# Optimization experiments

Measured on AMD Instinct MI355X. Metric: run time of the kernel, lower is better.

The kernel has to match this reference:

```python
import jax, jax.numpy as jnp
import numpy as np


def setup_inputs() -> dict:
    key = jax.random.key(0)
    ks = jax.random.split(key, 6)
    B, S, H = 1, 512, 2048
    NH, D = 16, 128
    S_CACHE = 8192
    TOPK = 16
    hidden_states = jax.random.normal(ks[0], (B, S, H), dtype=jnp.float32)
    Wqkv = jax.random.normal(ks[1], (3 * H, H), dtype=jnp.float32) * 0.02
    Wout = jax.random.normal(ks[2], (H, H), dtype=jnp.float32) * 0.02
    k_cache = jax.random.normal(ks[3], (B, NH, S_CACHE, D), dtype=jnp.float32)
    v_cache = jax.random.normal(ks[4], (B, NH, S_CACHE, D), dtype=jnp.float32)
    position_bias = jax.random.normal(ks[5], (NH, S, S), dtype=jnp.float32) * 0.1
    # causal mask: True = masked out (matches torch masked_fill semantics)
    attention_mask = ~jnp.tril(jnp.ones((S, S), dtype=bool))
    return {
        "hidden_states": hidden_states,
        "Wqkv": Wqkv,
        "Wout": Wout,
        "k_cache": k_cache,
        "v_cache": v_cache,
        "position_bias": position_bias,
        "attention_mask": attention_mask,
        "topk": TOPK,
    }


SIM_THRESHOLD = 0.25  # config.sim_threshold


def reference(hidden_states, Wqkv, Wout, k_cache, v_cache, position_bias,
              attention_mask, topk):
    B, S, H = hidden_states.shape
    NH, D = k_cache.shape[1], k_cache.shape[3]
    scale = 1.0 / jnp.sqrt(jnp.asarray(D, hidden_states.dtype))

    # QKV projection (Linear, no bias): x @ W^T, then split heads
    qkv = jnp.einsum('bsh,oh->bso', hidden_states, Wqkv)
    q, k, v = jnp.split(qkv, 3, axis=-1)
    def to_heads(x):
        return x.reshape(B, S, NH, D).transpose(0, 2, 1, 3)  # [B,NH,S,D]
    q, k, v = to_heads(q), to_heads(k), to_heads(v)

    # local attention scores + alibi-style bias
    scores_local = jnp.einsum('bhqd,bhkd->bhqk', q, k) * scale
    scores_local = scores_local + position_bias[None]  # [B,NH,S,S]

    # cosine-similarity retrieval over long-range cache
    q_n = q / jnp.linalg.norm(q, axis=-1, keepdims=True)
    k_n = k_cache / jnp.linalg.norm(k_cache, axis=-1, keepdims=True)
    sim = jnp.einsum('bhqd,bhkd->bhqk', q_n, k_n)  # [B,NH,S,S_CACHE]
    val, idx = jax.lax.top_k(sim, topk)            # [B,NH,S,topk]
    reshaped_idx = idx.reshape(B, NH, S * topk)

    # gather retrieved K/V
    sel_k = jnp.take_along_axis(k_cache, reshaped_idx[..., None], axis=2)  # [B,NH,S*topk,D]
    sel_v = jnp.take_along_axis(v_cache, reshaped_idx[..., None], axis=2)

    scores_cache = jnp.einsum('bhqd,bhkd->bhqk', q, sel_k) * scale  # [B,NH,S,S*topk]
    neg = jnp.finfo(scores_cache.dtype).min

    # similarity-threshold mask (mask_by_sim=True)
    sim_mask = ~(val > SIM_THRESHOLD)                       # [B,NH,S,topk]
    sim_mask = sim_mask.reshape(B, NH, 1, S * topk)         # broadcast over queries
    scores_cache = jnp.where(sim_mask, neg, scores_cache)

    # block-diagonal external-memory mask: query i attends only to its own topk slots
    rows = jnp.arange(S)[:, None]
    cols_block = jnp.arange(S * topk)[None, :] // topk
    ext_mask = cols_block != rows                           # [S, S*topk], True = masked

    full_mask = jnp.concatenate([ext_mask, attention_mask], axis=1)  # [S, S*topk+S]
    scores = jnp.concatenate([scores_cache, scores_local], axis=-1)
    scores = jnp.where(full_mask[None, None], neg, scores)

    attn = jax.nn.softmax(scores.astype(jnp.float32), axis=-1).astype(v.dtype)
    values = jnp.concatenate([sel_v, v], axis=2)            # [B,NH,S*topk+S,D]
    ctx = jnp.einsum('bhqk,bhkd->bhqd', attn, values)
    ctx = ctx.transpose(0, 2, 1, 3).reshape(B, S, H)
    attn_output = jnp.einsum('bsh,oh->bso', ctx, Wout)
    return attn_output
```

## Files before the change

### kernel.cpp

```cpp
#include <hip/hip_runtime.h>

typedef _Float16 half8 __attribute__((ext_vector_type(8)));
typedef _Float16 half4 __attribute__((ext_vector_type(4)));
typedef _Float16 half2t __attribute__((ext_vector_type(2)));
typedef float f32x4 __attribute__((ext_vector_type(4)));
typedef float f32x2 __attribute__((ext_vector_type(2)));

#define NHEAD 16
#define SEQ 512
#define DIM 128
#define HID 2048
#define SCACHE 8192
#define CAP 64
#define SCALE 0.08838834764831845f
#define NEG_INF (-__builtin_inff())
#define RECMAX 512

__global__ __launch_bounds__(256) void gemm_xwT(const float* __restrict__ A,
                                                const float* __restrict__ B,
                                                float* __restrict__ Cpart,
                                                int K, int gridN, int kslices) {
  __shared__ __align__(16) _Float16 As[128][84];
  __shared__ __align__(16) _Float16 Bs[128][84];
  int b = blockIdx.x;
  int kblk = b % kslices;
  int nm = b / kslices;
  int nblk = nm % gridN, mblk = nm / gridN;
  int N = gridN * 128;
  int kchunk = K / kslices;
  int t = threadIdx.x;
  int lane = t & 63, wid = t >> 6;
  int wm = (wid >> 1) * 64, wn = (wid & 1) * 64;
  f32x4 acc[4][4] = {};
  const float* Ab = A + (size_t)mblk * 128 * K;
  const float* Bb = B + (size_t)nblk * 128 * K;
  int rowS = t >> 4, c4 = (t & 15) * 4;

  for (int k0 = kblk * kchunk; k0 < kblk * kchunk + kchunk; k0 += 64) {
#pragma unroll
    for (int i = 0; i < 8; ++i) {
      int row = rowS + 16 * i;
      float4 av = *(const float4*)(Ab + (size_t)row * K + k0 + c4);
      float4 bv = *(const float4*)(Bb + (size_t)row * K + k0 + c4);
      half4 ah = {(_Float16)av.x, (_Float16)av.y, (_Float16)av.z, (_Float16)av.w};
      half4 bh = {(_Float16)bv.x, (_Float16)bv.y, (_Float16)bv.z, (_Float16)bv.w};
      *(half4*)&As[row][c4] = ah;
      *(half4*)&Bs[row][c4] = bh;
    }
    __syncthreads();
#pragma unroll
    for (int ks = 0; ks < 2; ++ks) {
      int ko = ks * 32 + (lane >> 4) * 8;
      int rr = lane & 15;
      half8 af[4], bf[4];
#pragma unroll
      for (int i = 0; i < 4; ++i) af[i] = *(const half8*)&As[wm + i * 16 + rr][ko];
#pragma unroll
      for (int j = 0; j < 4; ++j) bf[j] = *(const half8*)&Bs[wn + j * 16 + rr][ko];
#pragma unroll
      for (int i = 0; i < 4; ++i)
#pragma unroll
        for (int j = 0; j < 4; ++j)
          acc[i][j] = __builtin_amdgcn_mfma_f32_16x16x32_f16(af[i], bf[j], acc[i][j], 0, 0, 0);
    }
    __syncthreads();
  }
  float* Cp = Cpart + (size_t)kblk * ((size_t)gridN * 128) * 512;
  int cR = (lane >> 4) * 4, cC = lane & 15;
#pragma unroll
  for (int i = 0; i < 4; ++i)
#pragma unroll
    for (int j = 0; j < 4; ++j) {
      int row = mblk * 128 + wm + i * 16 + cR;
      int col = nblk * 128 + wn + j * 16 + cC;
#pragma unroll
      for (int r = 0; r < 4; ++r)
        Cp[(size_t)(row + r) * N + col] = acc[i][j][r];
    }
}

__global__ __launch_bounds__(256) void reduce_k(const float* __restrict__ part,
                                                float* __restrict__ dst,
                                                int kslices, int ncol, int dstride) {
  size_t e = ((size_t)blockIdx.x * 256 + threadIdx.x) * 4;
  size_t slice = (size_t)512 * ncol;
  f32x4 s = *(const f32x4*)(part + e);
  for (int p = 1; p < kslices; ++p)
    s += *(const f32x4*)(part + (size_t)p * slice + e);
  size_t row = e / ncol;
  int col = (int)(e % ncol);
  *(f32x4*)(dst + row * dstride + col) = s;
}

__global__ __launch_bounds__(256) void split_hilo(const float* __restrict__ src,
                                                  _Float16* __restrict__ hi,
                                                  _Float16* __restrict__ lo) {
  size_t e = ((size_t)blockIdx.x * 256 + threadIdx.x) * 4;
  f32x4 v = *(const f32x4*)(src + e);
  half4 h = {(_Float16)v[0], (_Float16)v[1], (_Float16)v[2], (_Float16)v[3]};
  half4 l = {(_Float16)(v[0] - (float)h[0]), (_Float16)(v[1] - (float)h[1]),
             (_Float16)(v[2] - (float)h[2]), (_Float16)(v[3] - (float)h[3])};
  *(half4*)(hi + e) = h;
  *(half4*)(lo + e) = l;
}

__global__ __launch_bounds__(256) void gemm_q_hi(const _Float16* __restrict__ Ahg,
                                                 const _Float16* __restrict__ Alg,
                                                 const _Float16* __restrict__ Bhg,
                                                 const _Float16* __restrict__ Blg,
                                                 float* __restrict__ C) {
  __shared__ __align__(16) _Float16 Ahs[32][72], Als[32][72];
  __shared__ __align__(16) _Float16 Bhs[32][72], Bls[32][72];
  int b = blockIdx.x;
  int nblk = b & 63, mblk = b >> 6;
  int t = threadIdx.x, lane = t & 63, w = t >> 6;
  int wm = (w >> 1) * 16, wn = (w & 1) * 16;
  int quad = lane >> 4, rr = lane & 15;
  f32x4 acc = {};
  const _Float16* Ab0 = Ahg + (size_t)(mblk * 32) * 2048;
  const _Float16* Ab1 = Alg + (size_t)(mblk * 32) * 2048;
  const _Float16* Bb0 = Bhg + (size_t)(nblk * 32) * 2048;
  const _Float16* Bb1 = Blg + (size_t)(nblk * 32) * 2048;
  int srow = t >> 3, sc = (t & 7) * 8;

  for (int k0 = 0; k0 < 2048; k0 += 64) {
    size_t goff = (size_t)srow * 2048 + k0 + sc;
    *(uint4*)&Ahs[srow][sc] = *(const uint4*)(Ab0 + goff);
    *(uint4*)&Als[srow][sc] = *(const uint4*)(Ab1 + goff);
    *(uint4*)&Bhs[srow][sc] = *(const uint4*)(Bb0 + goff);
    *(uint4*)&Bls[srow][sc] = *(const uint4*)(Bb1 + goff);
    __syncthreads();
#pragma unroll
    for (int ks = 0; ks < 2; ++ks) {
      int ko = ks * 32 + quad * 8;
      half8 afh = *(const half8*)&Ahs[wm + rr][ko];
      half8 afl = *(const half8*)&Als[wm + rr][ko];
      half8 bfh = *(const half8*)&Bhs[wn + rr][ko];
      half8 bfl = *(const half8*)&Bls[wn + rr][ko];
      acc = __builtin_amdgcn_mfma_f32_16x16x32_f16(afl, bfh, acc, 0, 0, 0);
      acc = __builtin_amdgcn_mfma_f32_16x16x32_f16(afh, bfl, acc, 0, 0, 0);
      acc = __builtin_amdgcn_mfma_f32_16x16x32_f16(afh, bfh, acc, 0, 0, 0);
    }
    __syncthreads();
  }
  int row = mblk * 32 + wm + quad * 4;
  int col = nblk * 32 + wn + rr;
#pragma unroll
  for (int r = 0; r < 4; ++r)
    C[(size_t)(row + r) * (3 * HID) + col] = acc[r];
}

__global__ __launch_bounds__(256) void cache_norm(const float* __restrict__ kc,
                                                  _Float16* __restrict__ kn16,
                                                  double* __restrict__ kninv) {
  int w = threadIdx.x >> 6, lane = threadIdx.x & 63;
  int row = blockIdx.x * 4 + w;
  f32x2 v = *(const f32x2*)(kc + (size_t)row * DIM + lane * 2);
  double s = (double)v[0] * v[0] + (double)v[1] * v[1];
#pragma unroll
  for (int off = 32; off; off >>= 1) s += __shfl_xor(s, off);
  float inv = rsqrtf((float)s);
  half2t o = {(_Float16)(v[0] * inv), (_Float16)(v[1] * inv)};
  *(half2t*)(kn16 + (size_t)row * DIM + lane * 2) = o;
  if (lane == 0) kninv[row] = 1.0 / sqrt(s);
}

__global__ __launch_bounds__(256) void prep_local(const float* __restrict__ qkv,
                                                  _Float16* __restrict__ q16,
                                                  _Float16* __restrict__ k16,
                                                  _Float16* __restrict__ qn16) {
  int w = threadIdx.x >> 6, lane = threadIdx.x & 63;
  int rid = blockIdx.x * 4 + w;
  int h = rid >> 9, s = rid & 511;
  const float* qp = qkv + (size_t)s * (3 * HID) + h * DIM + lane * 2;
  f32x2 q = *(const f32x2*)qp;
  f32x2 k = *(const f32x2*)(qp + HID);
  float ss = q[0] * q[0] + q[1] * q[1];
#pragma unroll
  for (int off = 32; off; off >>= 1) ss += __shfl_xor(ss, off);
  float inv = rsqrtf(ss);
  half2t qh = {(_Float16)q[0], (_Float16)q[1]};
  half2t kh = {(_Float16)k[0], (_Float16)k[1]};
  half2t qnh = {(_Float16)(q[0] * inv), (_Float16)(q[1] * inv)};
  *(half2t*)(q16 + (size_t)rid * DIM + lane * 2) = qh;
  *(half2t*)(k16 + (size_t)rid * DIM + lane * 2) = kh;
  *(half2t*)(qn16 + (size_t)rid * DIM + lane * 2) = qnh;
}

__global__ __launch_bounds__(256) void sim_cand(const _Float16* __restrict__ qn16,
                                                const _Float16* __restrict__ kn16,
                                                int* __restrict__ rec,
                                                int* __restrict__ reccnt) {
  __shared__ __align__(16) _Float16 As[128 * 128];
  __shared__ int ls_buf[RECMAX];
  __shared__ int ls_cnt;
  int b = blockIdx.x;
  int xcd = b & 7, slot = b >> 3;
  int mq = slot & 3;
  int p = (slot >> 2) * 8 + xcd;
  int h = p >> 6, nblk = p & 63;
  int t = threadIdx.x, lane = t & 63, w = t >> 6;
  int quad = lane >> 4, rr = lane & 15;
  if (t == 0) ls_cnt = 0;

  half8 bf[2][4];
  {
    const _Float16* kb = kn16 + ((size_t)(h * SCACHE + nblk * 128 + w * 32)) * DIM;
#pragma unroll
    for (int jn = 0; jn < 2; ++jn)
#pragma unroll
      for (int ks = 0; ks < 4; ++ks)
        bf[jn][ks] = *(const half8*)(kb + (size_t)(jn * 16 + rr) * DIM + ks * 32 + quad * 8);
  }

  {
    const _Float16* qA = qn16 + ((size_t)(h * SEQ + mq * 128)) * DIM;
    uint4 sreg[8];
#pragma unroll
    for (int i = 0; i < 8; ++i) {
      int f = t + 256 * i;
      sreg[i] = *(const uint4*)(qA + (size_t)(f >> 4) * DIM + (f & 15) * 8);
    }
#pragma unroll
    for (int i = 0; i < 8; ++i) {
      int f = t + 256 * i;
      int row = f >> 4, c = f & 15;
      *(uint4*)&As[row * DIM + ((c ^ (row & 7)) * 8)] = sreg[i];
    }
  }
  __syncthreads();

  f32x4 acc[8][2] = {};
#pragma unroll
  for (int i = 0; i < 8; ++i) {
    int R = i * 16 + rr;
    half8 af[4];
#pragma unroll
    for (int ks = 0; ks < 4; ++ks)
      af[ks] = *(const half8*)&As[R * DIM + (((ks * 4 + quad) ^ (rr & 7)) * 8)];
#pragma unroll
    for (int jn = 0; jn < 2; ++jn)
#pragma unroll
      for (int ks = 0; ks < 4; ++ks)
        acc[i][jn] = __builtin_amdgcn_mfma_f32_16x16x32_f16(af[ks], bf[jn][ks], acc[i][jn], 0, 0, 0);
  }

#pragma unroll
  for (int i = 0; i < 8; ++i)
#pragma unroll
    for (int jn = 0; jn < 2; ++jn)
#pragma unroll
      for (int r = 0; r < 4; ++r) {
        float v = acc[i][jn][r];
        if (v > 0.249f) {
          int q = mq * 128 + i * 16 + quad * 4 + r;
          int key = nblk * 128 + w * 32 + jn * 16 + rr;
          int pq = atomicAdd(&ls_cnt, 1);
          if (pq < RECMAX) ls_buf[pq] = (q << 13) | key;
        }
      }
  __syncthreads();
  int total = ls_cnt;
  if (total > RECMAX) total = RECMAX;
  int* rp = rec + (size_t)b * RECMAX;
  for (int e = t; e < total; e += 256) rp[e] = ls_buf[e];
  if (t == 0) reccnt[b] = total;
}

__global__ __launch_bounds__(256) void cand_merge(const int* __restrict__ rec,
                                                  const int* __restrict__ reccnt,
                                                  int* __restrict__ cnt,
                                                  int* __restrict__ cidx) {
  __shared__ int lc[128];
  __shared__ int pfx[65];
  __shared__ int bAs[64];
  int blk = blockIdx.x;
  int h = blk >> 2, mq = blk & 3;
  int t = threadIdx.x;
  if (t < 128) lc[t] = 0;
  if (t < 64) {
    int p = h * 64 + t;
    int bA = (p & 7) + 8 * (((p >> 3) << 2) + mq);
    bAs[t] = bA;
    pfx[t + 1] = reccnt[bA];
  }
  if (t == 0) pfx[0] = 0;
  __syncthreads();
  if (t == 0) {
    int s = 0;
    for (int i = 1; i <= 64; ++i) { s += pfx[i]; pfx[i] = s; }
  }
  __syncthreads();
  int T = pfx[64];

  for (int e0 = t; e0 < T; e0 += 512) {
    int e1 = e0 + 256;
    int lo0 = 0, hi0 = 64;
#pragma unroll
    for (int it = 0; it < 6; ++it) {
      int mid = (lo0 + hi0) >> 1;
      if (pfx[mid] <= e0) lo0 = mid; else hi0 = mid;
    }
    int lo1 = 0;
    if (e1 < T) {
      int hi1 = 64;
#pragma unroll
      for (int it = 0; it < 6; ++it) {
        int mid = (lo1 + hi1) >> 1;
        if (pfx[mid] <= e1) lo1 = mid; else hi1 = mid;
      }
    }
    int rv0 = rec[(size_t)bAs[lo0] * RECMAX + (e0 - pfx[lo0])];
    int rv1 = (e1 < T) ? rec[(size_t)bAs[lo1] * RECMAX + (e1 - pfx[lo1])] : 0;

    {
      int q = rv0 >> 13, key = rv0 & 8191;
      int pos = atomicAdd(&lc[q & 127], 1);
      if (pos < CAP) cidx[((size_t)h * 512 + q) * CAP + pos] = key;
    }
    if (e1 < T) {
      int q = rv1 >> 13, key = rv1 & 8191;
      int pos = atomicAdd(&lc[q & 127], 1);
      if (pos < CAP) cidx[((size_t)h * 512 + q) * CAP + pos] = key;
    }
  }
  __syncthreads();
  if (t < 128) cnt[h * 512 + mq * 128 + t] = lc[t];
}

__global__ __launch_bounds__(256) void select_topk(const int* __restrict__ cnt,
                                                   const int* __restrict__ cidx,
                                                   const float* __restrict__ qkv,
                                                   const float* __restrict__ kcache,
                                                   const double* __restrict__ kninv,
                                                   int* __restrict__ sel_idx,
                                                   float* __restrict__ sel_score) {
  int w = threadIdx.x >> 6, lane = threadIdx.x & 63;
  int rowid = blockIdx.x * 4 + w;
  int h = rowid >> 9, s = rowid & 511;
  const float* qp = qkv + (size_t)s * (3 * HID) + h * DIM;

  f32x2 qv2 = *(const f32x2*)(qp + lane * 2);
  double qs = (double)qv2[0] * qv2[0] + (double)qv2[1] * qv2[1];
#pragma unroll
  for (int off = 32; off; off >>= 1) qs += __shfl_xor(qs, off);
  double thr = 0.25 * sqrt(qs);

  int n = min(cnt[rowid], CAP);
  int idx = 0x7fffffff;
  double r = -1e300, d = 0.0;
  if (lane < n) {
    idx = cidx[rowid * CAP + lane];
    const float* kp = kcache + ((size_t)(h * SCACHE + idx)) * DIM;
    double d0 = 0.0, d1 = 0.0;
#pragma unroll
    for (int j = 0; j < DIM; j += 8) {
      f32x4 ka = *(const f32x4*)(kp + j);
      f32x4 kb = *(const f32x4*)(kp + j + 4);
      f32x4 qa = *(const f32x4*)(qp + j);
      f32x4 qb = *(const f32x4*)(qp + j + 4);
      d0 = fma((double)qa[0], (double)ka[0], d0);
      d1 = fma((double)qa[1], (double)ka[1], d1);
      d0 = fma((double)qa[2], (double)ka[2], d0);
      d1 = fma((double)qa[3], (double)ka[3], d1);
      d0 = fma((double)qb[0], (double)kb[0], d0);
      d1 = fma((double)qb[1], (double)kb[1], d1);
      d0 = fma((double)qb[2], (double)kb[2], d0);
      d1 = fma((double)qb[3], (double)kb[3], d1);
    }
    d = d0 + d1;
    r = d * kninv[h * SCACHE + idx];
  }

  int rank = 0;
  for (int j = 0; j < n; ++j) {
    double rj = __shfl(r, j);
    int ij = __shfl(idx, j);
    if (rj > r || (rj == r && ij < idx)) ++rank;
  }
  bool sel = (lane < n) && (rank < 16) && (r > thr);
  unsigned long long m = __ballot(sel);
  int nsel = __popcll(m);
  if (sel) {
    int pos = __popcll(m & ((1ull << lane) - 1));
    sel_idx[rowid * 16 + pos] = idx;
    sel_score[rowid * 16 + pos] = (float)(d * (double)SCALE);
  }
  if (lane >= nsel && lane < 16) {
    sel_idx[rowid * 16 + lane] = 0;
    sel_score[rowid * 16 + lane] = NEG_INF;
  }
}

__global__ __launch_bounds__(256) void attn_part(const float* __restrict__ qkv,
                                                 const _Float16* __restrict__ q16,
                                                 const _Float16* __restrict__ k16,
                                                 const float* __restrict__ bias,
                                                 float* __restrict__ part_m,
                                                 float* __restrict__ part_l,
                                                 float* __restrict__ part_o) {
  __shared__ __align__(16) _Float16 Vs[128][136];
  __shared__ __align__(16) _Float16 Ps[16][136];
  __shared__ float mred[16][4], lred[16][4];

  int pb = blockIdx.x;
  int tt = pb % 80, h = pb / 80;
  int qb, cb;
  if (tt < 8)       { qb = tt;                cb = 0; }
  else if (tt < 24) { int u = tt - 8;  qb = 8 + (u >> 1); cb = u & 1; }
  else if (tt < 48) { int u = tt - 24; int q3 = u / 3; qb = 16 + q3; cb = u - q3 * 3; }
  else              { int u = tt - 48; qb = 24 + (u >> 2); cb = u & 3; }
  int q0 = qb * 16, kc0 = cb * 128;

  int t = threadIdx.x, lane = t & 63, w = t >> 6;
  int quad = lane >> 4, col = lane & 15;

  const float* vbase = qkv + 2 * HID + h * DIM;
#pragma unroll
  for (int i = 0; i < 16; ++i) {
    int idx = t + 256 * i;
    int key = idx & 127, dg = idx >> 7;
    f32x4 vv = *(const f32x4*)(vbase + (size_t)(kc0 + key) * (3 * HID) + dg * 4);
#pragma unroll
    for (int e = 0; e < 4; ++e) Vs[dg * 4 + e][key] = (_Float16)vv[e];
  }

  const _Float16* qbp = q16 + ((size_t)(h * SEQ + q0)) * DIM;
  half8 af[4];
#pragma unroll
  for (int ks = 0; ks < 4; ++ks)
    af[ks] = *(const half8*)(qbp + (size_t)col * DIM + ks * 32 + quad * 8);

  f32x4 acc[2] = {};
#pragma unroll
  for (int jn = 0; jn < 2; ++jn) {
    const _Float16* kp = k16 + ((size_t)(h * SEQ + kc0 + w * 32 + jn * 16 + col)) * DIM;
#pragma unroll
    for (int ks = 0; ks < 4; ++ks) {
      half8 bf = *(const half8*)(kp + ks * 32 + quad * 8);
      acc[jn] = __builtin_amdgcn_mfma_f32_16x16x32_f16(af[ks], bf, acc[jn], 0, 0, 0);
    }
  }
  float s[2][4];
#pragma unroll
  for (int jn = 0; jn < 2; ++jn) {
    int keyg = kc0 + w * 32 + jn * 16 + col;
#pragma unroll
    for (int r = 0; r < 4; ++r) {
      int qrow = q0 + quad * 4 + r;
      float sv = NEG_INF;
      if (keyg <= qrow)
        sv = acc[jn][r] * SCALE + bias[((size_t)h * SEQ + qrow) * SEQ + keyg];
      s[jn][r] = sv;
    }
  }

  float mw[4];
#pragma unroll
  for (int r = 0; r < 4; ++r) {
    float m = fmaxf(s[0][r], s[1][r]);
#pragma unroll
    for (int off = 1; off < 16; off <<= 1) m = fmaxf(m, __shfl_xor(m, off));
    mw[r] = m;
  }
  if (col == 0)
#pragma unroll
    for (int r = 0; r < 4; ++r) mred[quad * 4 + r][w] = mw[r];
  __syncthreads();

  float M[4];
#pragma unroll
  for (int r = 0; r < 4; ++r) {
    int row = quad * 4 + r;
    float m = fmaxf(fmaxf(mred[row][0], mred[row][1]),
                    fmaxf(mred[row][2], mred[row][3]));
    M[r] = m;
    float p0 = __expf(s[0][r] - m);
    float p1 = __expf(s[1][r] - m);
    Ps[row][w * 32 + col] = (_Float16)p0;
    Ps[row][w * 32 + 16 + col] = (_Float16)p1;
    float l = p0 + p1;
#pragma unroll
    for (int off = 1; off < 16; off <<= 1) l += __shfl_xor(l, off);
    if (col == 0) lred[row][w] = l;
  }
  if (w == 0 && col == 0)
#pragma unroll
    for (int r = 0; r < 4; ++r) part_m[pb * 16 + quad * 4 + r] = M[r];
  __syncthreads();

  f32x4 o[2] = {};
#pragma unroll
  for (int jn = 0; jn < 2; ++jn) {
#pragma unroll
    for (int ks = 0; ks < 4; ++ks) {
      half8 a = *(const half8*)&Ps[col][ks * 32 + quad * 8];
      half8 bv = *(const half8*)&Vs[w * 32 + jn * 16 + col][ks * 32 + quad * 8];
      o[jn] = __builtin_amdgcn_mfma_f32_16x16x32_f16(a, bv, o[jn], 0, 0, 0);
    }
  }
#pragma unroll
  for (int jn = 0; jn < 2; ++jn)
#pragma unroll
    for (int r = 0; r < 4; ++r)
      part_o[((size_t)pb * 16 + quad * 4 + r) * 128 + w * 32 + jn * 16 + col] = o[jn][r];
  if (t < 16)
    part_l[pb * 16 + t] = lred[t][0] + lred[t][1] + lred[t][2] + lred[t][3];
}

__global__ __launch_bounds__(256) void attn_merge(const float* __restrict__ part_m,
                                                  const float* __restrict__ part_l,
                                                  const float* __restrict__ part_o,
                                                  const int* __restrict__ sel_idx,
                                                  const float* __restrict__ sel_score,
                                                  const float* __restrict__ vcache,
                                                  float* __restrict__ ctx) {
  int w = threadIdx.x >> 6, lane = threadIdx.x & 63;
  int row = blockIdx.x * 4 + w;
  int h = row >> 9, q = row & 511;
  int qb = q >> 4, r = q & 15;
  int base = (qb < 8) ? qb
           : (qb < 16) ? 8 + 2 * (qb - 8)
           : (qb < 24) ? 24 + 3 * (qb - 16)
                       : 48 + 4 * (qb - 24);
  int ncb = (qb >> 3) + 1;
  int pb0 = h * 80 + base;

  float scv[16], mc = NEG_INF;
#pragma unroll
  for (int j = 0; j < 16; ++j) {
    scv[j] = sel_score[row * 16 + j];
    mc = fmaxf(mc, scv[j]);
  }
  float mi[4];
  float M = mc;
  for (int i = 0; i < ncb; ++i) {
    mi[i] = part_m[(pb0 + i) * 16 + r];
    M = fmaxf(M, mi[i]);
  }
  f32x2 O = {0.f, 0.f};
  float L = 0.f;
  for (int i = 0; i < ncb; ++i) {
    float sc = __expf(mi[i] - M);
    f32x2 ov = *(const f32x2*)(part_o + ((size_t)(pb0 + i) * 16 + r) * 128 + lane * 2);
    O += ov * sc;
    L += part_l[(pb0 + i) * 16 + r] * sc;
  }
#pragma unroll
  for (int j = 0; j < 16; ++j) {
    if (scv[j] > NEG_INF) {
      float wv = __expf(scv[j] - M);
      int idx = sel_idx[row * 16 + j];
      f32x2 v = *(const f32x2*)(vcache + ((size_t)(h * SCACHE + idx)) * DIM + lane * 2);
      O += v * wv;
      L += wv;
    }
  }
  f32x2 res = O * (1.f / L);
  *(f32x2*)(ctx + (size_t)q * HID + h * DIM + lane * 2) = res;
}

extern "C" void kernel_launch(void* const* d_in, const int* in_sizes, int n_in,
                              void* d_out, int out_size, void* d_ws, size_t ws_size,
                              hipStream_t stream) {
  const float* hidden = (const float*)d_in[0];
  const float* Wqkv   = (const float*)d_in[1];
  const float* Wout   = (const float*)d_in[2];
  const float* kcache = (const float*)d_in[3];
  const float* vcache = (const float*)d_in[4];
  const float* bias   = (const float*)d_in[5];

  char* ws = (char*)d_ws;
  size_t off = 0;
  float*    qkv   = (float*)(ws + off);    off += (size_t)SEQ * 3 * HID * 4;
  _Float16* q16   = (_Float16*)(ws + off); off += (size_t)NHEAD * SEQ * DIM * 2;
  _Float16* k16   = (_Float16*)(ws + off); off += (size_t)NHEAD * SEQ * DIM * 2;
  _Float16* qn16  = (_Float16*)(ws + off); off += (size_t)NHEAD * SEQ * DIM * 2;
  _Float16* kn16  = (_Float16*)(ws + off); off += (size_t)NHEAD * SCACHE * DIM * 2;
  double*   kninv = (double*)(ws + off);   off += (size_t)NHEAD * SCACHE * 8;
  int*      ccnt  = (int*)(ws + off);      off += (size_t)NHEAD * SEQ * 4;
  int*      cidx  = (int*)(ws + off);      off += (size_t)NHEAD * SEQ * CAP * 4;
  int*      selidx  = (int*)(ws + off);    off += (size_t)NHEAD * SEQ * 16 * 4;
  float*    selsc   = (float*)(ws + off);  off += (size_t)NHEAD * SEQ * 16 * 4;
  float*    ctx   = (float*)(ws + off);    off += (size_t)SEQ * HID * 4;
  float*    pm    = (float*)(ws + off);    off += (size_t)1280 * 16 * 4;
  float*    pl    = (float*)(ws + off);    off += (size_t)1280 * 16 * 4;
  float*    po    = (float*)(ws + off);    off += (size_t)1280 * 16 * 128 * 4;
  int*      rec    = (int*)po;
  int*      reccnt = rec + (size_t)4096 * RECMAX;
  float*    gpart = (float*)(ws + off);
  _Float16* Ahg = (_Float16*)gpart;
  _Float16* Alg = Ahg + (size_t)SEQ * HID;
  _Float16* Bhg = Alg + (size_t)SEQ * HID;
  _Float16* Blg = Bhg + (size_t)HID * HID;

  cache_norm<<<dim3(NHEAD * SCACHE / 4), dim3(256), 0, stream>>>(kcache, kn16, kninv);
  gemm_xwT<<<dim3(4 * 32 * 4), dim3(256), 0, stream>>>(hidden, Wqkv + (size_t)2048 * 2048,
                                                       gpart, 2048, 32, 4);
  reduce_k<<<dim3(SEQ * 4096 / 1024), dim3(256), 0, stream>>>(gpart, qkv + 2048, 4, 4096,
                                                              3 * HID);
  split_hilo<<<dim3(SEQ * HID / 1024), dim3(256), 0, stream>>>(hidden, Ahg, Alg);
  split_hilo<<<dim3(HID * HID / 1024), dim3(256), 0, stream>>>(Wqkv, Bhg, Blg);
  gemm_q_hi<<<dim3(1024), dim3(256), 0, stream>>>(Ahg, Alg, Bhg, Blg, qkv);
  prep_local<<<dim3(NHEAD * SEQ / 4), dim3(256), 0, stream>>>(qkv, q16, k16, qn16);
  sim_cand<<<dim3(4096), dim3(256), 0, stream>>>(qn16, kn16, rec, reccnt);
  cand_merge<<<dim3(64), dim3(256), 0, stream>>>(rec, reccnt, ccnt, cidx);
  select_topk<<<dim3(NHEAD * SEQ / 4), dim3(256), 0, stream>>>(ccnt, cidx, qkv, kcache,
                                                               kninv, selidx, selsc);
  attn_part<<<dim3(16 * 80), dim3(256), 0, stream>>>(qkv, q16, k16, bias, pm, pl, po);
  attn_merge<<<dim3(NHEAD * SEQ / 4), dim3(256), 0, stream>>>(pm, pl, po, selidx, selsc,
                                                              vcache, ctx);
  gemm_xwT<<<dim3(4 * 16 * 8), dim3(256), 0, stream>>>(ctx, Wout, gpart, 2048, 16, 8);
  reduce_k<<<dim3(SEQ * 2048 / 1024), dim3(256), 0, stream>>>(gpart, (float*)d_out, 8, 2048,
                                                              2048);
}
```

Before: 419.2 us.

## Process four key tiles per sim_cand block with prefetched B fragments

Each sim_cand block now covers 512 cache keys instead of 128, so the Q tile staged in shared memory is reused across four key tiles. The next tile's K fragments are prefetched into registers while the current tile runs its MFMAs. Threshold hits are gathered into a bitmask and walked with ctz instead of 64 branched atomics. The grid shrinks 4x and RECMAX doubles, with cand_merge updated to merge 16 records per head-quarter; the costs are fewer blocks for latency hiding and more register pressure.

```diff
diff --git a/kernel.cpp b/kernel.cpp
--- a/kernel.cpp
+++ b/kernel.cpp
@@ -14,7 +14,7 @@
 #define CAP 64
 #define SCALE 0.08838834764831845f
 #define NEG_INF (-__builtin_inff())
-#define RECMAX 512
+#define RECMAX 1024
 
 __global__ __launch_bounds__(256) void gemm_xwT(const float* __restrict__ A,
                                                 const float* __restrict__ B,
@@ -198,20 +198,23 @@
   int xcd = b & 7, slot = b >> 3;
   int mq = slot & 3;
   int p = (slot >> 2) * 8 + xcd;
-  int h = p >> 6, nblk = p & 63;
+  int h = p >> 4, g = p & 15;
   int t = threadIdx.x, lane = t & 63, w = t >> 6;
   int quad = lane >> 4, rr = lane & 15;
   if (t == 0) ls_cnt = 0;
 
-  half8 bf[2][4];
-  {
-    const _Float16* kb = kn16 + ((size_t)(h * SCACHE + nblk * 128 + w * 32)) * DIM;
+  const _Float16* kbase = kn16 + (size_t)h * SCACHE * DIM
+                        + (size_t)(g * 512 + w * 32 + rr) * DIM + quad * 8;
+  auto loadB = [&](half8 (&dst)[2][4], int tt) {
 #pragma unroll
     for (int jn = 0; jn < 2; ++jn)
 #pragma unroll
       for (int ks = 0; ks < 4; ++ks)
-        bf[jn][ks] = *(const half8*)(kb + (size_t)(jn * 16 + rr) * DIM + ks * 32 + quad * 8);
-  }
+        dst[jn][ks] = *(const half8*)(kbase + (size_t)(tt * 128 + jn * 16) * DIM + ks * 32);
+  };
+
+  half8 bf[2][4], bn[2][4];
+  loadB(bf, 0);
 
   {
     const _Float16* qA = qn16 + ((size_t)(h * SEQ + mq * 128)) * DIM;
@@ -230,35 +233,51 @@
   }
   __syncthreads();
 
-  f32x4 acc[8][2] = {};
-#pragma unroll
-  for (int i = 0; i < 8; ++i) {
-    int R = i * 16 + rr;
-    half8 af[4];
-#pragma unroll
-    for (int ks = 0; ks < 4; ++ks)
-      af[ks] = *(const half8*)&As[R * DIM + (((ks * 4 + quad) ^ (rr & 7)) * 8)];
-#pragma unroll
-    for (int jn = 0; jn < 2; ++jn)
+#pragma unroll
+  for (int tt = 0; tt < 4; ++tt) {
+    if (tt < 3) loadB(bn, tt + 1);
+
+    f32x4 acc[8][2] = {};
+#pragma unroll
+    for (int i = 0; i < 8; ++i) {
+      int R = i * 16 + rr;
+      half8 af[4];
 #pragma unroll
       for (int ks = 0; ks < 4; ++ks)
-        acc[i][jn] = __builtin_amdgcn_mfma_f32_16x16x32_f16(af[ks], bf[jn][ks], acc[i][jn], 0, 0, 0);
-  }
-
-#pragma unroll
-  for (int i = 0; i < 8; ++i)
-#pragma unroll
-    for (int jn = 0; jn < 2; ++jn)
-#pragma unroll
-      for (int r = 0; r < 4; ++r) {
-        float v = acc[i][jn][r];
-        if (v > 0.249f) {
-          int q = mq * 128 + i * 16 + quad * 4 + r;
-          int key = nblk * 128 + w * 32 + jn * 16 + rr;
-          int pq = atomicAdd(&ls_cnt, 1);
-          if (pq < RECMAX) ls_buf[pq] = (q << 13) | key;
-        }
-      }
+        af[ks] = *(const half8*)&As[R * DIM + (((ks * 4 + quad) ^ (rr & 7)) * 8)];
+#pragma unroll
+      for (int jn = 0; jn < 2; ++jn)
+#pragma unroll
+        for (int ks = 0; ks < 4; ++ks)
+          acc[i][jn] = __builtin_amdgcn_mfma_f32_16x16x32_f16(af[ks], bf[jn][ks], acc[i][jn], 0, 0, 0);
+    }
+
+    unsigned long long hm = 0ull;
+#pragma unroll
+    for (int i = 0; i < 8; ++i)
+#pragma unroll
+      for (int jn = 0; jn < 2; ++jn)
+#pragma unroll
+        for (int r = 0; r < 4; ++r)
+          hm |= (unsigned long long)(acc[i][jn][r] > 0.249f) << (i * 8 + jn * 4 + r);
+    int key_base = (g * 4 + tt) * 128 + w * 32 + rr;
+    while (hm) {
+      int bit = __builtin_ctzll(hm);
+      hm &= hm - 1;
+      int i = bit >> 3, jn = (bit >> 2) & 1, r = bit & 3;
+      int q = mq * 128 + i * 16 + (quad << 2) + r;
+      int pq = atomicAdd(&ls_cnt, 1);
+      if (pq < RECMAX) ls_buf[pq] = (q << 13) | (key_base + jn * 16);
+    }
+
+    if (tt < 3) {
+#pragma unroll
+      for (int jn = 0; jn < 2; ++jn)
+#pragma unroll
+        for (int ks = 0; ks < 4; ++ks)
+          bf[jn][ks] = bn[jn][ks];
+    }
+  }
   __syncthreads();
   int total = ls_cnt;
   if (total > RECMAX) total = RECMAX;
@@ -272,14 +291,14 @@
                                                   int* __restrict__ cnt,
                                                   int* __restrict__ cidx) {
   __shared__ int lc[128];
-  __shared__ int pfx[65];
-  __shared__ int bAs[64];
+  __shared__ int pfx[17];
+  __shared__ int bAs[16];
   int blk = blockIdx.x;
   int h = blk >> 2, mq = blk & 3;
   int t = threadIdx.x;
   if (t < 128) lc[t] = 0;
-  if (t < 64) {
-    int p = h * 64 + t;
+  if (t < 16) {
+    int p = h * 16 + t;
     int bA = (p & 7) + 8 * (((p >> 3) << 2) + mq);
     bAs[t] = bA;
     pfx[t + 1] = reccnt[bA];
@@ -288,24 +307,24 @@
   __syncthreads();
   if (t == 0) {
     int s = 0;
-    for (int i = 1; i <= 64; ++i) { s += pfx[i]; pfx[i] = s; }
+    for (int i = 1; i <= 16; ++i) { s += pfx[i]; pfx[i] = s; }
   }
   __syncthreads();
-  int T = pfx[64];
+  int T = pfx[16];
 
   for (int e0 = t; e0 < T; e0 += 512) {
     int e1 = e0 + 256;
-    int lo0 = 0, hi0 = 64;
-#pragma unroll
-    for (int it = 0; it < 6; ++it) {
+    int lo0 = 0, hi0 = 16;
+#pragma unroll
+    for (int it = 0; it < 4; ++it) {
       int mid = (lo0 + hi0) >> 1;
       if (pfx[mid] <= e0) lo0 = mid; else hi0 = mid;
     }
     int lo1 = 0;
     if (e1 < T) {
-      int hi1 = 64;
-#pragma unroll
-      for (int it = 0; it < 6; ++it) {
+      int hi1 = 16;
+#pragma unroll
+      for (int it = 0; it < 4; ++it) {
         int mid = (lo1 + hi1) >> 1;
         if (pfx[mid] <= e1) lo1 = mid; else hi1 = mid;
       }
@@ -587,7 +606,7 @@
   float*    pl    = (float*)(ws + off);    off += (size_t)1280 * 16 * 4;
   float*    po    = (float*)(ws + off);    off += (size_t)1280 * 16 * 128 * 4;
   int*      rec    = (int*)po;
-  int*      reccnt = rec + (size_t)4096 * RECMAX;
+  int*      reccnt = rec + (size_t)1024 * RECMAX;
   float*    gpart = (float*)(ws + off);
   _Float16* Ahg = (_Float16*)gpart;
   _Float16* Alg = Ahg + (size_t)SEQ * HID;
@@ -603,7 +622,7 @@
   split_hilo<<<dim3(HID * HID / 1024), dim3(256), 0, stream>>>(Wqkv, Bhg, Blg);
   gemm_q_hi<<<dim3(1024), dim3(256), 0, stream>>>(Ahg, Alg, Bhg, Blg, qkv);
   prep_local<<<dim3(NHEAD * SEQ / 4), dim3(256), 0, stream>>>(qkv, q16, k16, qn16);
-  sim_cand<<<dim3(4096), dim3(256), 0, stream>>>(qn16, kn16, rec, reccnt);
+  sim_cand<<<dim3(1024), dim3(256), 0, stream>>>(qn16, kn16, rec, reccnt);
   cand_merge<<<dim3(64), dim3(256), 0, stream>>>(rec, reccnt, ccnt, cidx);
   select_topk<<<dim3(NHEAD * SEQ / 4), dim3(256), 0, stream>>>(ccnt, cidx, qkv, kcache,
                                                                kninv, selidx, selsc);
```

Result: no change. 412.9 us (-1.5%).
